# Kernel tuning notes

Hardware: AMD Instinct MI355X
Metric: run time of the kernel (lower is better)

## Reference

```python
import jax, jax.numpy as jnp
import numpy as np

N = 3072
R = 16
B = 16


def setup_inputs() -> dict:
    key = jax.random.key(0)
    k1, k2, k3, k4, k5 = jax.random.split(key, 5)
    z1 = jax.random.normal(k1, (N, R), dtype=jnp.float32)
    z2 = jax.random.normal(k2, (N, R), dtype=jnp.float32)
    seg_matrix = jax.random.randint(k3, (N, N), 0, 2).astype(jnp.float32)
    cls_label = jax.random.randint(k4, (N,), 0, 30).astype(jnp.int64)
    batch = jnp.sort(jax.random.randint(k5, (N,), 0, B)).astype(jnp.int64)
    return {"z1": z1, "z2": z2, "seg_matrix": seg_matrix,
            "cls_label": cls_label, "batch": batch}


def reference(z1, z2, seg_matrix, cls_label, batch):
    n, r = z1.shape
    # seg_matrix += eye(N): self-pairs never have seg == 0
    seg = seg_matrix + jnp.eye(n, dtype=seg_matrix.dtype)
    # nodes with class labels 24/25/26 are excluded
    node_mask = (cls_label != 24) & (cls_label != 25) & (cls_label != 26)
    # pair (i, j) is written iff both nodes valid, same graph, and seg[i,j] == 0.
    # (the per-batch meshgrid/nonzero loop == same-batch pair condition)
    pair = (node_mask[:, None] & node_mask[None, :]
            & (batch[:, None] == batch[None, :])
            & (seg == 0.0))                              # [N, N]
    # default value: one-hot on relation 0 (concat of ones and zeros)
    default = jax.nn.one_hot(0, r, dtype=z1.dtype)        # [R]
    prod = z1[:, None, :] * z2[None, :, :]                # [N, N, R]
    return jnp.where(pair[:, :, None], prod, default)
```

## Files before the change

### kernel.cpp

```cpp
#include <hip/hip_runtime.h>
#include <cstddef>

#define NN 3072
#define RR 16
#define NB 16
#define UNROLL 8

typedef float f32x4 __attribute__((ext_vector_type(4)));

__global__ void frd_prep_kernel(const int* __restrict__ cls,
                                const int* __restrict__ batch,
                                int* __restrict__ key,
                                int* __restrict__ start) {
    int t = blockIdx.x * blockDim.x + threadIdx.x;
    if (t < NN) {
        int c = cls[t];
        int b = batch[t];
        key[t] = (c != 24 && c != 25 && c != 26) ? b : -1;
        int prev = (t == 0) ? -1 : batch[t - 1];
        for (int bb = prev + 1; bb <= b; ++bb) start[bb] = t;
        if (t == NN - 1)
            for (int bb = b + 1; bb <= NB; ++bb) start[bb] = NN;
    }
}

__global__ __launch_bounds__(256)
void frd_fill_kernel(const int* __restrict__ key, float* __restrict__ out) {
    const int base = blockIdx.x * (256 * UNROLL) + threadIdx.x;
    const int q = threadIdx.x & 3;
    const f32x4 val = {(q == 0) ? 1.0f : 0.0f, 0.0f, 0.0f, 0.0f};

#pragma unroll
    for (int k = 0; k < UNROLL; ++k) {
        const int idx = base + k * 256;
        const int pair = idx >> 2;
        const int i = pair / NN;
        const int j = pair - i * NN;
        const int ki = key[i];
        const int kj = key[j];
        const bool skip = (ki >= 0) && (ki == kj);
        if (!skip)
            __builtin_nontemporal_store(val, reinterpret_cast<f32x4*>(out + (size_t)idx * 4));
    }
}

__global__ __launch_bounds__(256)
void frd_diag_kernel(const float* __restrict__ z1,
                     const float* __restrict__ z2,
                     const float* __restrict__ seg,
                     const int* __restrict__ key,
                     const int* __restrict__ start,
                     float* __restrict__ out) {
    const int i = blockIdx.x;
    const int ki = key[i];
    if (ki < 0) return;
    const int s0 = start[ki];
    const int s1 = start[ki + 1];
    const int q = threadIdx.x & 3;
    const int g = threadIdx.x >> 2;

    const float4 a = *reinterpret_cast<const float4*>(z1 + i * RR + q * 4);
    const float d0 = (q == 0) ? 1.0f : 0.0f;

    for (int j = s0 + g; j < s1; j += 64) {
        if (key[j] != ki) continue;
        const float s = seg[i * NN + j];
        const float seg_eff = s + ((i == j) ? 1.0f : 0.0f);
        float* op = out + ((size_t)i * NN + j) * RR + q * 4;
        f32x4 r;
        if (seg_eff == 0.0f) {
            const float4 b = *reinterpret_cast<const float4*>(z2 + j * RR + q * 4);
            r.x = a.x * b.x; r.y = a.y * b.y; r.z = a.z * b.z; r.w = a.w * b.w;
        } else {
            r.x = d0; r.y = 0.0f; r.z = 0.0f; r.w = 0.0f;
        }
        __builtin_nontemporal_store(r, reinterpret_cast<f32x4*>(op));
    }
}

extern "C" void kernel_launch(void* const* d_in, const int* in_sizes, int n_in,
                              void* d_out, int out_size, void* d_ws, size_t ws_size,
                              hipStream_t stream) {
    const float* z1  = (const float*)d_in[0];
    const float* z2  = (const float*)d_in[1];
    const float* seg = (const float*)d_in[2];
    const int* cls   = (const int*)d_in[3];
    const int* batch = (const int*)d_in[4];
    float* out = (float*)d_out;
    int* key   = (int*)d_ws;
    int* start = key + NN;

    frd_prep_kernel<<<(NN + 255) / 256, 256, 0, stream>>>(cls, batch, key, start);
    const int total = NN * NN * 4;
    frd_fill_kernel<<<total / (256 * UNROLL), 256, 0, stream>>>(key, out);
    frd_diag_kernel<<<NN, 256, 0, stream>>>(z1, z2, seg, key, start, out);
}
```

Before: 126.7 us.

## Unconditionally fill defaults with grid-stride stores, diag writes only product pairs

The fill kernel no longer reads node keys or divides indices; it writes the one-hot default over the whole output with a fixed grid-stride loop, and it is launched before the prep kernel. The diag kernel now stores only pairs whose seg value is zero, relying on the earlier fill for all other pairs. This removes the per-element key lookups and division, but same-batch default pairs are now written twice, and the fill uses regular instead of nontemporal stores.

```diff
diff --git a/kernel.cpp b/kernel.cpp
--- a/kernel.cpp
+++ b/kernel.cpp
@@ -4,7 +4,8 @@
 #define NN 3072
 #define RR 16
 #define NB 16
-#define UNROLL 8
+#define FILL_BLOCKS 2048
+#define FILL_ITERS 72
 
 typedef float f32x4 __attribute__((ext_vector_type(4)));
 
@@ -25,22 +26,16 @@
 }
 
 __global__ __launch_bounds__(256)
-void frd_fill_kernel(const int* __restrict__ key, float* __restrict__ out) {
-    const int base = blockIdx.x * (256 * UNROLL) + threadIdx.x;
-    const int q = threadIdx.x & 3;
-    const f32x4 val = {(q == 0) ? 1.0f : 0.0f, 0.0f, 0.0f, 0.0f};
-
-#pragma unroll
-    for (int k = 0; k < UNROLL; ++k) {
-        const int idx = base + k * 256;
-        const int pair = idx >> 2;
-        const int i = pair / NN;
-        const int j = pair - i * NN;
-        const int ki = key[i];
-        const int kj = key[j];
-        const bool skip = (ki >= 0) && (ki == kj);
-        if (!skip)
-            __builtin_nontemporal_store(val, reinterpret_cast<f32x4*>(out + (size_t)idx * 4));
+void frd_fill_kernel(float* __restrict__ out) {
+    const int t = blockIdx.x * 256 + threadIdx.x;
+    const float d0 = ((t & 3) == 0) ? 1.0f : 0.0f;
+    const f32x4 r = {d0, 0.0f, 0.0f, 0.0f};
+    float* p = out + (size_t)t * 4;
+    const size_t step = (size_t)FILL_BLOCKS * 256 * 4;
+#pragma unroll 4
+    for (int it = 0; it < FILL_ITERS; ++it) {
+        *reinterpret_cast<f32x4*>(p) = r;
+        p += step;
     }
 }
 
@@ -60,20 +55,16 @@
     const int g = threadIdx.x >> 2;
 
     const float4 a = *reinterpret_cast<const float4*>(z1 + i * RR + q * 4);
-    const float d0 = (q == 0) ? 1.0f : 0.0f;
 
     for (int j = s0 + g; j < s1; j += 64) {
         if (key[j] != ki) continue;
         const float s = seg[i * NN + j];
         const float seg_eff = s + ((i == j) ? 1.0f : 0.0f);
+        if (seg_eff != 0.0f) continue;
+        const float4 b = *reinterpret_cast<const float4*>(z2 + j * RR + q * 4);
+        f32x4 r;
+        r.x = a.x * b.x; r.y = a.y * b.y; r.z = a.z * b.z; r.w = a.w * b.w;
         float* op = out + ((size_t)i * NN + j) * RR + q * 4;
-        f32x4 r;
-        if (seg_eff == 0.0f) {
-            const float4 b = *reinterpret_cast<const float4*>(z2 + j * RR + q * 4);
-            r.x = a.x * b.x; r.y = a.y * b.y; r.z = a.z * b.z; r.w = a.w * b.w;
-        } else {
-            r.x = d0; r.y = 0.0f; r.z = 0.0f; r.w = 0.0f;
-        }
         __builtin_nontemporal_store(r, reinterpret_cast<f32x4*>(op));
     }
 }
@@ -90,8 +81,7 @@
     int* key   = (int*)d_ws;
     int* start = key + NN;
 
+    frd_fill_kernel<<<FILL_BLOCKS, 256, 0, stream>>>(out);
     frd_prep_kernel<<<(NN + 255) / 256, 256, 0, stream>>>(cls, batch, key, start);
-    const int total = NN * NN * 4;
-    frd_fill_kernel<<<total / (256 * UNROLL), 256, 0, stream>>>(key, out);
     frd_diag_kernel<<<NN, 256, 0, stream>>>(z1, z2, seg, key, start, out);
 }
```

New measurement: 156.0 us. 1.23x slower.

## Fuse fill and diagonal-block kernels into one launch with persistent grid-stride fill

Applied to the files above, without the earlier changes.

Merges the default-value fill kernel and the same-graph pair kernel into a single launch. The first 256 blocks fill the output with a grid-stride loop, and the remaining blocks each handle one row of the same-batch region. This removes a kernel launch and the serialization between fill and diagonal work, so both can overlap. The risk is that only 256 fill blocks may not saturate write bandwidth for the roughly 600MB output.

```diff
diff --git a/kernel.cpp b/kernel.cpp
--- a/kernel.cpp
+++ b/kernel.cpp
@@ -4,7 +4,8 @@
 #define NN 3072
 #define RR 16
 #define NB 16
-#define UNROLL 8
+#define FILL_BLOCKS 256
+#define FILL_ITERS 576
 
 typedef float f32x4 __attribute__((ext_vector_type(4)));
 
@@ -25,56 +26,57 @@
 }
 
 __global__ __launch_bounds__(256)
-void frd_fill_kernel(const int* __restrict__ key, float* __restrict__ out) {
-    const int base = blockIdx.x * (256 * UNROLL) + threadIdx.x;
-    const int q = threadIdx.x & 3;
-    const f32x4 val = {(q == 0) ? 1.0f : 0.0f, 0.0f, 0.0f, 0.0f};
+void frd_fused_kernel(const float* __restrict__ z1,
+                      const float* __restrict__ z2,
+                      const float* __restrict__ seg,
+                      const int* __restrict__ key,
+                      const int* __restrict__ start,
+                      float* __restrict__ out) {
+    const int bid = blockIdx.x;
+    if (bid < FILL_BLOCKS) {
+        const int t = bid * 256 + threadIdx.x;
+        const float d0 = ((t & 3) == 0) ? 1.0f : 0.0f;
+        const f32x4 r = {d0, 0.0f, 0.0f, 0.0f};
+        int quad = t;
+        const int step = FILL_BLOCKS * 256;
+#pragma unroll 8
+        for (int it = 0; it < FILL_ITERS; ++it) {
+            const int pair = quad >> 2;
+            const int i = pair / NN;
+            const int j = pair - i * NN;
+            const int ki = key[i];
+            const int kj = key[j];
+            const bool skip = (ki >= 0) && (ki == kj);
+            if (!skip)
+                __builtin_nontemporal_store(r, reinterpret_cast<f32x4*>(out + (size_t)quad * 4));
+            quad += step;
+        }
+    } else {
+        const int i = bid - FILL_BLOCKS;
+        const int ki = key[i];
+        if (ki < 0) return;
+        const int s0 = start[ki];
+        const int s1 = start[ki + 1];
+        const int q = threadIdx.x & 3;
+        const int g = threadIdx.x >> 2;
 
-#pragma unroll
-    for (int k = 0; k < UNROLL; ++k) {
-        const int idx = base + k * 256;
-        const int pair = idx >> 2;
-        const int i = pair / NN;
-        const int j = pair - i * NN;
-        const int ki = key[i];
-        const int kj = key[j];
-        const bool skip = (ki >= 0) && (ki == kj);
-        if (!skip)
-            __builtin_nontemporal_store(val, reinterpret_cast<f32x4*>(out + (size_t)idx * 4));
-    }
-}
+        const float4 a = *reinterpret_cast<const float4*>(z1 + i * RR + q * 4);
+        const float d0 = (q == 0) ? 1.0f : 0.0f;
 
-__global__ __launch_bounds__(256)
-void frd_diag_kernel(const float* __restrict__ z1,
-                     const float* __restrict__ z2,
-                     const float* __restrict__ seg,
-                     const int* __restrict__ key,
-                     const int* __restrict__ start,
-                     float* __restrict__ out) {
-    const int i = blockIdx.x;
-    const int ki = key[i];
-    if (ki < 0) return;
-    const int s0 = start[ki];
-    const int s1 = start[ki + 1];
-    const int q = threadIdx.x & 3;
-    const int g = threadIdx.x >> 2;
-
-    const float4 a = *reinterpret_cast<const float4*>(z1 + i * RR + q * 4);
-    const float d0 = (q == 0) ? 1.0f : 0.0f;
-
-    for (int j = s0 + g; j < s1; j += 64) {
-        if (key[j] != ki) continue;
-        const float s = seg[i * NN + j];
-        const float seg_eff = s + ((i == j) ? 1.0f : 0.0f);
-        float* op = out + ((size_t)i * NN + j) * RR + q * 4;
-        f32x4 r;
-        if (seg_eff == 0.0f) {
-            const float4 b = *reinterpret_cast<const float4*>(z2 + j * RR + q * 4);
-            r.x = a.x * b.x; r.y = a.y * b.y; r.z = a.z * b.z; r.w = a.w * b.w;
-        } else {
-            r.x = d0; r.y = 0.0f; r.z = 0.0f; r.w = 0.0f;
+        for (int j = s0 + g; j < s1; j += 64) {
+            if (key[j] != ki) continue;
+            const float s = seg[i * NN + j];
+            const float seg_eff = s + ((i == j) ? 1.0f : 0.0f);
+            f32x4 r;
+            if (seg_eff == 0.0f) {
+                const float4 b = *reinterpret_cast<const float4*>(z2 + j * RR + q * 4);
+                r.x = a.x * b.x; r.y = a.y * b.y; r.z = a.z * b.z; r.w = a.w * b.w;
+            } else {
+                r.x = d0; r.y = 0.0f; r.z = 0.0f; r.w = 0.0f;
+            }
+            float* op = out + ((size_t)i * NN + j) * RR + q * 4;
+            __builtin_nontemporal_store(r, reinterpret_cast<f32x4*>(op));
         }
-        __builtin_nontemporal_store(r, reinterpret_cast<f32x4*>(op));
     }
 }
 
@@ -91,7 +93,5 @@
     int* start = key + NN;
 
     frd_prep_kernel<<<(NN + 255) / 256, 256, 0, stream>>>(cls, batch, key, start);
-    const int total = NN * NN * 4;
-    frd_fill_kernel<<<total / (256 * UNROLL), 256, 0, stream>>>(key, out);
-    frd_diag_kernel<<<NN, 256, 0, stream>>>(z1, z2, seg, key, start, out);
+    frd_fused_kernel<<<FILL_BLOCKS + NN, 256, 0, stream>>>(z1, z2, seg, key, start, out);
 }
```

Result: faster. 120.3 us (-5.1%).
